# Optimization experiments

Hardware: AMD Instinct MI355X
Metric: run time of the kernel (lower is better)

Reference implementation:

```python
import jax, jax.numpy as jnp
import numpy as np
from jax import lax

# db1 (Haar) decomposition filters per pywt: dec_lo=[s,s], dec_hi=[-s,s], s=1/sqrt(2).
# pywt mode='zero' DWT == full zero-padded convolution downsampled at odd indices,
# which for filter length f equals strided correlation (stride 2) with the FLIPPED
# filter and padding (f-2, f-1). For Haar f=2: padding (0, 1).
_S = np.float32(0.7071067811865476)
# kernel [out_ch=2, in_ch=1, flen=2]; rows are flipped dec_lo and flipped dec_hi
_KERNEL = jnp.array([[[_S, _S]], [[_S, -_S]]], dtype=jnp.float32)


def _dwt_step(x):
    """One Haar DWT level. x: [B, 1, L] -> (cA [B,1,ceil((L+1)/2)], cD same)."""
    y = lax.conv_general_dilated(
        x, _KERNEL, window_strides=(2,), padding=[(0, 1)],
        dimension_numbers=("NCH", "OIH", "NCH"))
    return y[:, 0:1, :], y[:, 1:2, :]


def setup_inputs() -> dict:
    key = jax.random.key(0)
    B, L = 2048, 16384
    x = jax.random.normal(key, (B, L), dtype=jnp.float32)
    return {"x": x}


def reference(x):
    """Returns (cA3, cD3, cD2, cD1), each [B, 1, L/2^k] — matching pywt.wavedec order."""
    if x.ndim == 2:
        x = x[:, None, :]
    level = 3
    cA = x
    details = []
    for _ in range(level):
        cA, cD = _dwt_step(cA)
        details.append(cD)
    return (cA, *details[::-1])
```

## Files before the change

kernel.cpp:

```cpp
#include <hip/hip_runtime.h>


#define HS 0.7071067811865476f

constexpr int B = 2048;
constexpr int L = 16384;
constexpr int GROUPS_PER_ROW = L / 8;
constexpr int TOTAL_UNITS = B * GROUPS_PER_ROW;

__global__ __launch_bounds__(256) void haar3_kernel(const float* __restrict__ x,
                                                    float* __restrict__ out) {
    const int u = blockIdx.x * 256 + threadIdx.x;
    const int row = u >> 11;
    const int pos = u & 2047;

    const float4* xin = (const float4*)(x + ((size_t)row << 14) + ((size_t)pos << 3));
    const float4 v0 = xin[0];
    const float4 v1 = xin[1];

    const float a10 = HS * (v0.x + v0.y), d10 = HS * (v0.x - v0.y);
    const float a11 = HS * (v0.z + v0.w), d11 = HS * (v0.z - v0.w);
    const float a12 = HS * (v1.x + v1.y), d12 = HS * (v1.x - v1.y);
    const float a13 = HS * (v1.z + v1.w), d13 = HS * (v1.z - v1.w);
    const float a20 = HS * (a10 + a11), d20 = HS * (a10 - a11);
    const float a21 = HS * (a12 + a13), d21 = HS * (a12 - a13);
    const float a3 = HS * (a20 + a21), d3 = HS * (a20 - a21);

    float* cA3 = out;
    float* cD3 = out + (size_t)B * 2048;
    float* cD2 = out + (size_t)B * 2048 * 2;
    float* cD1 = out + (size_t)B * 2048 * 2 + (size_t)B * 4096;

    const size_t rp = ((size_t)row << 11) + pos;
    cA3[rp] = a3;
    cD3[rp] = d3;
    ((float2*)cD2)[rp] = make_float2(d20, d21);
    ((float4*)cD1)[rp] = make_float4(d10, d11, d12, d13);
}

extern "C" void kernel_launch(void* const* d_in, const int* in_sizes, int n_in,
                              void* d_out, int out_size, void* d_ws, size_t ws_size,
                              hipStream_t stream) {
    const float* x = (const float*)d_in[0];
    float* out = (float*)d_out;
    constexpr int block = 256;
    constexpr int grid = TOTAL_UNITS / block;
    haar3_kernel<<<grid, block, 0, stream>>>(x, out);
}
```

Measured before the change: 230.5 us.

## Process one float4 per thread with wave shuffle and nontemporal loads/stores

Each thread now handles four input samples instead of eight and pairs with a neighbouring lane via a cross-lane shuffle to finish the third Haar level. All global loads and stores use nontemporal builtins to avoid polluting caches on this streaming workload. This doubles the thread count and leaves half the lanes idle for the level-3 stores, in exchange for simpler addressing and cache-bypassing memory traffic.

```diff
diff --git a/kernel.cpp b/kernel.cpp
--- a/kernel.cpp
+++ b/kernel.cpp
@@ -3,47 +3,45 @@
 
 #define HS 0.7071067811865476f
 
+typedef float vf4 __attribute__((ext_vector_type(4)));
+typedef float vf2 __attribute__((ext_vector_type(2)));
+
 constexpr int B = 2048;
 constexpr int L = 16384;
-constexpr int GROUPS_PER_ROW = L / 8;
-constexpr int TOTAL_UNITS = B * GROUPS_PER_ROW;
+constexpr int UNITS = B * (L / 4);
+constexpr size_t OFF_CD3 = (size_t)B * 2048;
+constexpr size_t OFF_CD2 = OFF_CD3 * 2;
+constexpr size_t OFF_CD1 = OFF_CD2 + (size_t)B * 4096;
 
-__global__ __launch_bounds__(256) void haar3_kernel(const float* __restrict__ x,
+__global__ __launch_bounds__(256) void haar3_kernel(const vf4* __restrict__ x4,
                                                     float* __restrict__ out) {
     const int u = blockIdx.x * 256 + threadIdx.x;
-    const int row = u >> 11;
-    const int pos = u & 2047;
+    const int pos = u & 4095;
 
-    const float4* xin = (const float4*)(x + ((size_t)row << 14) + ((size_t)pos << 3));
-    const float4 v0 = xin[0];
-    const float4 v1 = xin[1];
+    const vf4 v = __builtin_nontemporal_load(&x4[u]);
 
-    const float a10 = HS * (v0.x + v0.y), d10 = HS * (v0.x - v0.y);
-    const float a11 = HS * (v0.z + v0.w), d11 = HS * (v0.z - v0.w);
-    const float a12 = HS * (v1.x + v1.y), d12 = HS * (v1.x - v1.y);
-    const float a13 = HS * (v1.z + v1.w), d13 = HS * (v1.z - v1.w);
-    const float a20 = HS * (a10 + a11), d20 = HS * (a10 - a11);
-    const float a21 = HS * (a12 + a13), d21 = HS * (a12 - a13);
-    const float a3 = HS * (a20 + a21), d3 = HS * (a20 - a21);
+    const float a10 = HS * (v.x + v.y), d10 = HS * (v.x - v.y);
+    const float a11 = HS * (v.z + v.w), d11 = HS * (v.z - v.w);
+    const float a2 = HS * (a10 + a11), d2 = HS * (a10 - a11);
 
-    float* cA3 = out;
-    float* cD3 = out + (size_t)B * 2048;
-    float* cD2 = out + (size_t)B * 2048 * 2;
-    float* cD1 = out + (size_t)B * 2048 * 2 + (size_t)B * 4096;
+    vf2 d1v; d1v.x = d10; d1v.y = d11;
+    __builtin_nontemporal_store(d1v, ((vf2*)(out + OFF_CD1)) + u);
+    __builtin_nontemporal_store(d2, out + OFF_CD2 + u);
 
-    const size_t rp = ((size_t)row << 11) + pos;
-    cA3[rp] = a3;
-    cD3[rp] = d3;
-    ((float2*)cD2)[rp] = make_float2(d20, d21);
-    ((float4*)cD1)[rp] = make_float4(d10, d11, d12, d13);
+    const float a2p = __shfl_xor(a2, 1);
+    if ((pos & 1) == 0) {
+        const int rp3 = u >> 1;
+        __builtin_nontemporal_store(HS * (a2 + a2p), out + rp3);
+        __builtin_nontemporal_store(HS * (a2 - a2p), out + OFF_CD3 + rp3);
+    }
 }
 
 extern "C" void kernel_launch(void* const* d_in, const int* in_sizes, int n_in,
                               void* d_out, int out_size, void* d_ws, size_t ws_size,
                               hipStream_t stream) {
-    const float* x = (const float*)d_in[0];
+    const vf4* x4 = (const vf4*)d_in[0];
     float* out = (float*)d_out;
     constexpr int block = 256;
-    constexpr int grid = TOTAL_UNITS / block;
-    haar3_kernel<<<grid, block, 0, stream>>>(x, out);
+    constexpr int grid = UNITS / block;
+    haar3_kernel<<<grid, block, 0, stream>>>(x4, out);
 }
```

Result: faster. 216.0 us (-6.3%).
